# Kernel tuning notes

Hardware: AMD Instinct MI355X
Metric: run time of the kernel (lower is better)

The kernel has to match this reference:

```python
import jax, jax.numpy as jnp
import numpy as np

N_NODES = 100000


def _gcn_norm(edge_index, edge_weight, num_nodes):
    # add self loops with weight 1 (PyG GCNConv default)
    loop = jnp.arange(num_nodes, dtype=edge_index.dtype)
    src = jnp.concatenate([edge_index[0], loop])
    dst = jnp.concatenate([edge_index[1], loop])
    w = jnp.concatenate([edge_weight, jnp.ones(num_nodes, edge_weight.dtype)])
    deg = jax.ops.segment_sum(w, dst, num_segments=num_nodes)
    dinv = jnp.where(deg > 0, jax.lax.rsqrt(deg), 0.0).astype(edge_weight.dtype)
    norm = dinv[src] * w * dinv[dst]
    return src, dst, norm


def _gcn_conv(x, W, b, src, dst, norm):
    h = x @ W                                   # [N, out]
    msg = h[src] * norm[:, None]                # [E+N, out] gather + scale
    out = jax.ops.segment_sum(msg, dst, num_segments=x.shape[0])
    return out + b


def setup_inputs() -> dict:
    key = jax.random.key(0)
    ks = jax.random.split(key, 6)
    nfeat, nhid, nclass, E = 128, 64, 40, 1600000
    return {
        "x": jax.random.normal(ks[0], (N_NODES, nfeat), jnp.float32),
        "edge_index": jax.random.randint(ks[1], (2, E), 0, N_NODES, jnp.int64),
        "edge_weight": jax.random.uniform(ks[2], (E,), jnp.float32),
        "W1": jax.random.normal(ks[3], (nfeat, nhid), jnp.float32) / np.sqrt(nfeat),
        "b1": jnp.zeros((nhid,), jnp.float32),
        "W2": jax.random.normal(ks[4], (nhid, nclass), jnp.float32) / np.sqrt(nhid),
        "b2": jnp.zeros((nclass,), jnp.float32),
    }


def reference(x, edge_index, edge_weight, W1, b1, W2, b2):
    src, dst, norm = _gcn_norm(edge_index, edge_weight, x.shape[0])
    h = jax.nn.relu(_gcn_conv(x, W1, b1, src, dst, norm))
    # dropout p=0.0 / eval mode -> identity
    h = _gcn_conv(h, W2, b2, src, dst, norm)
    return jax.nn.log_softmax(h, axis=1)
```

## Files before the change

kernel.cpp:

```cpp
#include <hip/hip_runtime.h>
#include <hip/hip_fp16.h>
#include <math.h>

#define NFEAT 128
#define NHID 64
#define NCLASS 40
#define BNODES 256
#define BSHIFT 8
#define EPB 4096
#define CAPSH 13
#define CAP (1 << CAPSH)
#define LCAP 5120

typedef _Float16 f16x8 __attribute__((ext_vector_type(8)));
typedef float f32x4 __attribute__((ext_vector_type(4)));

static __device__ __forceinline__ __half2 i2h2(int x) { union { int i; __half2 h; } u; u.i = x; return u.h; }
static __device__ __forceinline__ int h22i(__half2 h) { union { int i; __half2 h; } u; u.h = h; return u.i; }
static __device__ __forceinline__ __half2 shfl_xor_h2(__half2 v, int off) { return i2h2(__shfl_xor(h22i(v), off)); }


__global__ void k_init(int* __restrict__ gcur, int NB) {
    int i = blockIdx.x * blockDim.x + threadIdx.x;
    if (i < NB) gcur[i] = i << CAPSH;
}

__global__ __launch_bounds__(256) void k_bscatter(const int* __restrict__ src, const int* __restrict__ dst,
                                                  const float* __restrict__ w, int* __restrict__ gcur,
                                                  int2* __restrict__ csrT, int E, int NB) {
    __shared__ int2 sorted[EPB];
    __shared__ int gidx[EPB];
    __shared__ int lcnt[512], lscan[512], fb[512], lpos[512];
    int t = threadIdx.x;
    for (int i = t; i < 512; i += 256) { lcnt[i] = 0; lpos[i] = 0; }
    __syncthreads();
    int base = blockIdx.x * EPB;
    int rs[16], rd[16]; float rw[16];
    #pragma unroll
    for (int j = 0; j < 4; j++) {
        int e0 = base + j * 1024 + t * 4;
        if (e0 + 3 < E) {
            int4 s4 = *(const int4*)(src + e0);
            int4 d4 = *(const int4*)(dst + e0);
            float4 w4 = *(const float4*)(w + e0);
            rs[j * 4 + 0] = s4.x; rs[j * 4 + 1] = s4.y; rs[j * 4 + 2] = s4.z; rs[j * 4 + 3] = s4.w;
            rd[j * 4 + 0] = d4.x; rd[j * 4 + 1] = d4.y; rd[j * 4 + 2] = d4.z; rd[j * 4 + 3] = d4.w;
            rw[j * 4 + 0] = w4.x; rw[j * 4 + 1] = w4.y; rw[j * 4 + 2] = w4.z; rw[j * 4 + 3] = w4.w;
        } else {
            #pragma unroll
            for (int k = 0; k < 4; k++) {
                int e = e0 + k;
                bool ok = (e < E);
                rd[j * 4 + k] = ok ? dst[e] : -1;
                rs[j * 4 + k] = ok ? src[e] : 0;
                rw[j * 4 + k] = ok ? w[e] : 0.f;
            }
        }
    }
    #pragma unroll
    for (int i = 0; i < 16; i++)
        if (rd[i] >= 0) atomicAdd(&lcnt[rd[i] >> BSHIFT], 1);
    __syncthreads();
    int i0 = t, i1 = t + 256;
    lscan[i0] = lcnt[i0]; lscan[i1] = lcnt[i1];
    __syncthreads();
    for (int off = 1; off < 512; off <<= 1) {
        int v0 = (i0 >= off) ? lscan[i0 - off] : 0;
        int v1 = (i1 >= off) ? lscan[i1 - off] : 0;
        __syncthreads();
        lscan[i0] += v0; lscan[i1] += v1;
        __syncthreads();
    }
    for (int i = t; i < NB; i += 256) {
        int c = lcnt[i];
        if (c) {
            int gb = atomicAdd(&gcur[i], c);
            fb[i] = gb - (lscan[i] - c);
        }
    }
    __syncthreads();
    #pragma unroll
    for (int i = 0; i < 16; i++) {
        if (rd[i] >= 0) {
            int d = rd[i];
            int b = d >> BSHIFT;
            int p = (lscan[b] - lcnt[b]) + atomicAdd(&lpos[b], 1);
            int2 v;
            v.x = rs[i] | ((d & (BNODES - 1)) << 20);
            v.y = __float_as_int(rw[i]);
            sorted[p] = v;
            gidx[p] = fb[b] + p;
        }
    }
    __syncthreads();
    int tot = lscan[511];
    for (int i = t; i < tot; i += 256) csrT[gidx[i]] = sorted[i];
}

__global__ __launch_bounds__(256) void k_lsort(const int* __restrict__ gcur,
                                               int2* csr,
                                               int* __restrict__ offs, int* __restrict__ endo,
                                               float* __restrict__ dinv, int N) {
    __shared__ int2 sorted[LCAP];
    __shared__ int lh[BNODES];
    __shared__ int lo[BNODES];
    __shared__ float da[BNODES];
    int b = blockIdx.x, t = threadIdx.x;
    int rbase = b << CAPSH;
    int cnt = gcur[b] - rbase;
    if (cnt > LCAP) cnt = LCAP;
    lh[t] = 0; da[t] = 0.f;
    __syncthreads();
    int2 reg[20];
    #pragma unroll
    for (int i = 0; i < 20; i++) {
        int e = t + i * 256;
        reg[i] = (e < cnt) ? csr[rbase + e] : make_int2(-1, 0);
    }
    #pragma unroll
    for (int i = 0; i < 20; i++) {
        if (reg[i].x >= 0) {
            int dl = (reg[i].x >> 20) & 255;
            atomicAdd(&lh[dl], 1);
            atomicAdd(&da[dl], __int_as_float(reg[i].y));
        }
    }
    __syncthreads();
    int own = lh[t];
    lo[t] = own;
    __syncthreads();
    for (int off = 1; off < 256; off <<= 1) {
        int v = (t >= off) ? lo[t - off] : 0;
        __syncthreads();
        lo[t] += v;
        __syncthreads();
    }
    int excl = lo[t] - own;
    __syncthreads();
    lh[t] = excl;
    int gn = (b << BSHIFT) + t;
    if (gn < N) {
        offs[gn] = rbase + excl;
        endo[gn] = rbase + excl + own;
        dinv[gn] = rsqrtf(1.0f + da[t]);
    }
    __syncthreads();
    #pragma unroll
    for (int i = 0; i < 20; i++) {
        if (reg[i].x >= 0) {
            int dl = (reg[i].x >> 20) & 255;
            int p = atomicAdd(&lh[dl], 1);
            sorted[p] = reg[i];
        }
    }
    __syncthreads();
    for (int e = t; e < cnt; e += 256) {
        int2 v = sorted[e];
        __half2 w2 = __half2half2(__float2half(__int_as_float(v.y)));
        v.x &= 0xFFFFF;
        v.y = h22i(w2);
        csr[rbase + e] = v;
    }
}


__global__ __launch_bounds__(256) void k_gemm1(const float* __restrict__ x,
                                               const float* __restrict__ W,
                                               const float* __restrict__ dinv,
                                               __half* __restrict__ h, int N) {
    __shared__ _Float16 xh[64][136];
    __shared__ _Float16 Wt[64][136];
    int t = threadIdx.x;
    int row0 = blockIdx.x * 64;
    for (int i = t; i < 2048; i += 256) {
        int r = i >> 5, k4 = i & 31;
        int row = row0 + r;
        float4 v = (row < N) ? ((const float4*)(x + (size_t)row * NFEAT))[k4]
                             : make_float4(0.f, 0.f, 0.f, 0.f);
        *(__half2*)&xh[r][k4 * 4]     = __floats2half2_rn(v.x, v.y);
        *(__half2*)&xh[r][k4 * 4 + 2] = __floats2half2_rn(v.z, v.w);
    }
    for (int i = t; i < 4096; i += 256) {
        int k2 = i >> 6, c = i & 63;
        float a0 = W[(size_t)(2 * k2) * NHID + c];
        float a1 = W[(size_t)(2 * k2 + 1) * NHID + c];
        *(__half2*)&Wt[c][k2 * 2] = __floats2half2_rn(a0, a1);
    }
    __syncthreads();
    int wave = t >> 6, lane = t & 63;
    int quad = lane >> 4, l16 = lane & 15;
    int r0 = wave * 16;
    f32x4 acc[4] = {};
    #pragma unroll
    for (int k0 = 0; k0 < 128; k0 += 32) {
        f16x8 af = *(const f16x8*)&xh[r0 + l16][k0 + quad * 8];
        #pragma unroll
        for (int ct = 0; ct < 4; ct++) {
            f16x8 bf = *(const f16x8*)&Wt[ct * 16 + l16][k0 + quad * 8];
            acc[ct] = __builtin_amdgcn_mfma_f32_16x16x32_f16(af, bf, acc[ct], 0, 0, 0);
        }
    }
    #pragma unroll
    for (int ct = 0; ct < 4; ct++) {
        #pragma unroll
        for (int j = 0; j < 4; j++) {
            int row = row0 + r0 + quad * 4 + j;
            if (row < N)
                h[(size_t)row * NHID + ct * 16 + l16] = __float2half(dinv[row] * acc[ct][j]);
        }
    }
}


__global__ __launch_bounds__(256) void k_agg1(const int* __restrict__ offs, const int* __restrict__ endo,
                                              const int2* __restrict__ csr,
                                              const __half* __restrict__ h1, const float* __restrict__ dinv,
                                              const float* __restrict__ b1, __half* __restrict__ out1, int N) {
    int n = (blockIdx.x * blockDim.x + threadIdx.x) >> 6;
    if (n >= N) return;
    int lane = threadIdx.x & 63;
    int grp = lane >> 3;
    int c8 = lane & 7;
    const char* hb = (const char*)h1;
    unsigned int c16 = (unsigned int)c8 << 4;
    int e = offs[n], end = endo[n];
    float di = dinv[n];
    float4 hsv = *(const float4*)(hb + (unsigned int)n * 128u + c16);
    float4 bb0 = ((const float4*)b1)[2 * c8];
    float4 bb1 = ((const float4*)b1)[2 * c8 + 1];
    __half2 z = __floats2half2_rn(0.f, 0.f);
    __half2 aa0[4] = {z, z, z, z}, aa1[4] = {z, z, z, z};
    __half2 aa2[4] = {z, z, z, z}, aa3[4] = {z, z, z, z};
    {
        int2 v0, v1, v2, v3;
        int i0 = e + grp, i1 = e + 8 + grp, i2 = e + 16 + grp, i3 = e + 24 + grp;
        bool b0 = i0 < end, b1v = i1 < end, b2 = i2 < end, b3 = i3 < end;
        v0 = csr[b0 ? i0 : e];
        v1 = csr[b1v ? i1 : e];
        v2 = csr[b2 ? i2 : e];
        v3 = csr[b3 ? i3 : e];
        unsigned int r0 = b0 ? (unsigned int)(v0.x & 0xFFFFF) : 0u;
        unsigned int r1 = b1v ? (unsigned int)(v1.x & 0xFFFFF) : 0u;
        unsigned int r2 = b2 ? (unsigned int)(v2.x & 0xFFFFF) : 0u;
        unsigned int r3 = b3 ? (unsigned int)(v3.x & 0xFFFFF) : 0u;
        float4 h0 = *(const float4*)(hb + r0 * 128u + c16);
        float4 h1v = *(const float4*)(hb + r1 * 128u + c16);
        float4 h2v = *(const float4*)(hb + r2 * 128u + c16);
        float4 h3v = *(const float4*)(hb + r3 * 128u + c16);
        __half2 w0 = b0 ? i2h2(v0.y) : z;
        __half2 w1 = b1v ? i2h2(v1.y) : z;
        __half2 w2 = b2 ? i2h2(v2.y) : z;
        __half2 w3 = b3 ? i2h2(v3.y) : z;
        const __half2* p0 = (const __half2*)&h0;
        const __half2* p1 = (const __half2*)&h1v;
        const __half2* p2 = (const __half2*)&h2v;
        const __half2* p3 = (const __half2*)&h3v;
        #pragma unroll
        for (int q = 0; q < 4; q++) {
            aa0[q] = __hfma2(w0, p0[q], aa0[q]);
            aa1[q] = __hfma2(w1, p1[q], aa1[q]);
            aa2[q] = __hfma2(w2, p2[q], aa2[q]);
            aa3[q] = __hfma2(w3, p3[q], aa3[q]);
        }
    }
    for (int idx = e + 32 + grp; idx < end; idx += 8) {
        int2 v = csr[idx];
        unsigned int row = (unsigned int)(v.x & 0xFFFFF);
        float4 hv = *(const float4*)(hb + row * 128u + c16);
        __half2 wv = i2h2(v.y);
        const __half2* p = (const __half2*)&hv;
        #pragma unroll
        for (int q = 0; q < 4; q++) aa0[q] = __hfma2(wv, p[q], aa0[q]);
    }
    __half2 acc2[4];
    #pragma unroll
    for (int q = 0; q < 4; q++)
        acc2[q] = __hadd2(__hadd2(aa0[q], aa1[q]), __hadd2(aa2[q], aa3[q]));
    #pragma unroll
    for (int off = 8; off <= 32; off <<= 1) {
        #pragma unroll
        for (int q = 0; q < 4; q++) acc2[q] = __hadd2(acc2[q], shfl_xor_h2(acc2[q], off));
    }
    if (grp == 0) {
        float a[8], s[8];
        #pragma unroll
        for (int q = 0; q < 4; q++) {
            float2 fa = __half22float2(acc2[q]);
            a[2 * q] = fa.x; a[2 * q + 1] = fa.y;
            float2 f = __half22float2(((const __half2*)&hsv)[q]);
            s[2 * q] = f.x; s[2 * q + 1] = f.y;
        }
        float o[8];
        o[0] = fmaxf(di * (a[0] + s[0]) + bb0.x, 0.f);
        o[1] = fmaxf(di * (a[1] + s[1]) + bb0.y, 0.f);
        o[2] = fmaxf(di * (a[2] + s[2]) + bb0.z, 0.f);
        o[3] = fmaxf(di * (a[3] + s[3]) + bb0.w, 0.f);
        o[4] = fmaxf(di * (a[4] + s[4]) + bb1.x, 0.f);
        o[5] = fmaxf(di * (a[5] + s[5]) + bb1.y, 0.f);
        o[6] = fmaxf(di * (a[6] + s[6]) + bb1.z, 0.f);
        o[7] = fmaxf(di * (a[7] + s[7]) + bb1.w, 0.f);
        float4 st;
        #pragma unroll
        for (int q = 0; q < 4; q++)
            ((__half2*)&st)[q] = __floats2half2_rn(o[2 * q], o[2 * q + 1]);
        ((float4*)out1)[(size_t)n * 8 + c8] = st;
    }
}


__global__ __launch_bounds__(256) void k_gemm2(const __half* __restrict__ a,
                                               const float* __restrict__ W,
                                               const float* __restrict__ dinv,
                                               __half* __restrict__ h, int N) {
    __shared__ _Float16 As[64][72];
    __shared__ _Float16 Bt[64][72];
    int t = threadIdx.x;
    int row0 = blockIdx.x * 64;
    for (int i = t; i < 512; i += 256) {
        int r = i >> 3, q = i & 7;
        int row = row0 + r;
        f16x8 v = {};
        if (row < N) v = *(const f16x8*)(a + (size_t)row * NHID + q * 8);
        *(f16x8*)&As[r][q * 8] = v;
    }
    for (int i = t; i < 4096; i += 256) {
        int c = i >> 6, k = i & 63;
        float wv = (c < NCLASS) ? W[k * NCLASS + c] : 0.f;
        Bt[c][k] = (_Float16)wv;
    }
    __syncthreads();
    int wave = t >> 6, lane = t & 63;
    int quad = lane >> 4, l16 = lane & 15;
    int r0 = wave * 16;
    f32x4 acc[4] = {};
    #pragma unroll
    for (int k0 = 0; k0 < 64; k0 += 32) {
        f16x8 af = *(const f16x8*)&As[r0 + l16][k0 + quad * 8];
        #pragma unroll
        for (int ct = 0; ct < 4; ct++) {
            f16x8 bf = *(const f16x8*)&Bt[ct * 16 + l16][k0 + quad * 8];
            acc[ct] = __builtin_amdgcn_mfma_f32_16x16x32_f16(af, bf, acc[ct], 0, 0, 0);
        }
    }
    #pragma unroll
    for (int ct = 0; ct < 4; ct++) {
        int col = ct * 16 + l16;
        #pragma unroll
        for (int j = 0; j < 4; j++) {
            int row = row0 + r0 + quad * 4 + j;
            if (row < N)
                h[((size_t)row << 6) + col] = __float2half(dinv[row] * acc[ct][j]);
        }
    }
}


__global__ __launch_bounds__(256) void k_agg2(const int* __restrict__ offs, const int* __restrict__ endo,
                                              const int2* __restrict__ csr,
                                              const __half* __restrict__ h2, const float* __restrict__ dinv,
                                              const float* __restrict__ b2, float* __restrict__ out, int N) {
    int n = (blockIdx.x * blockDim.x + threadIdx.x) >> 6;
    if (n >= N) return;
    int lane = threadIdx.x & 63;
    int grp = lane >> 3;
    int c8 = lane & 7;
    const char* hb = (const char*)h2;
    unsigned int c16 = (unsigned int)c8 << 4;
    int e = offs[n], end = endo[n];
    bool act = (c8 < 5);
    float di = dinv[n];
    float4 hsv = *(const float4*)(hb + ((unsigned int)n << 7) + c16);
    float4 bb0 = {}, bb1 = {};
    if (act) {
        bb0 = ((const float4*)b2)[2 * c8];
        bb1 = ((const float4*)b2)[2 * c8 + 1];
    }
    __half2 z = __floats2half2_rn(0.f, 0.f);
    __half2 aa0[4] = {z, z, z, z}, aa1[4] = {z, z, z, z};
    __half2 aa2[4] = {z, z, z, z}, aa3[4] = {z, z, z, z};
    {
        int2 v0, v1, v2, v3;
        int i0 = e + grp, i1 = e + 8 + grp, i2 = e + 16 + grp, i3 = e + 24 + grp;
        bool b0 = i0 < end, b1v = i1 < end, b2c = i2 < end, b3 = i3 < end;
        v0 = csr[b0 ? i0 : e];
        v1 = csr[b1v ? i1 : e];
        v2 = csr[b2c ? i2 : e];
        v3 = csr[b3 ? i3 : e];
        unsigned int r0 = b0 ? (unsigned int)(v0.x & 0xFFFFF) : 0u;
        unsigned int r1 = b1v ? (unsigned int)(v1.x & 0xFFFFF) : 0u;
        unsigned int r2 = b2c ? (unsigned int)(v2.x & 0xFFFFF) : 0u;
        unsigned int r3 = b3 ? (unsigned int)(v3.x & 0xFFFFF) : 0u;
        float4 h0 = *(const float4*)(hb + (r0 << 7) + c16);
        float4 h1v = *(const float4*)(hb + (r1 << 7) + c16);
        float4 h2v = *(const float4*)(hb + (r2 << 7) + c16);
        float4 h3v = *(const float4*)(hb + (r3 << 7) + c16);
        __half2 w0 = b0 ? i2h2(v0.y) : z;
        __half2 w1 = b1v ? i2h2(v1.y) : z;
        __half2 w2 = b2c ? i2h2(v2.y) : z;
        __half2 w3 = b3 ? i2h2(v3.y) : z;
        const __half2* p0 = (const __half2*)&h0;
        const __half2* p1 = (const __half2*)&h1v;
        const __half2* p2 = (const __half2*)&h2v;
        const __half2* p3 = (const __half2*)&h3v;
        #pragma unroll
        for (int q = 0; q < 4; q++) {
            aa0[q] = __hfma2(w0, p0[q], aa0[q]);
            aa1[q] = __hfma2(w1, p1[q], aa1[q]);
            aa2[q] = __hfma2(w2, p2[q], aa2[q]);
            aa3[q] = __hfma2(w3, p3[q], aa3[q]);
        }
    }
    for (int idx = e + 32 + grp; idx < end; idx += 8) {
        int2 v = csr[idx];
        unsigned int row = (unsigned int)(v.x & 0xFFFFF);
        float4 hv = *(const float4*)(hb + (row << 7) + c16);
        __half2 wv = i2h2(v.y);
        const __half2* p = (const __half2*)&hv;
        #pragma unroll
        for (int q = 0; q < 4; q++) aa0[q] = __hfma2(wv, p[q], aa0[q]);
    }
    __half2 acc2[4];
    #pragma unroll
    for (int q = 0; q < 4; q++)
        acc2[q] = __hadd2(__hadd2(aa0[q], aa1[q]), __hadd2(aa2[q], aa3[q]));
    #pragma unroll
    for (int off = 8; off <= 32; off <<= 1) {
        #pragma unroll
        for (int q = 0; q < 4; q++) acc2[q] = __hadd2(acc2[q], shfl_xor_h2(acc2[q], off));
    }
    float a[8], s[8];
    #pragma unroll
    for (int q = 0; q < 4; q++) {
        float2 fa = __half22float2(acc2[q]);
        a[2 * q] = fa.x; a[2 * q + 1] = fa.y;
        float2 f = __half22float2(((const __half2*)&hsv)[q]);
        s[2 * q] = f.x; s[2 * q + 1] = f.y;
    }
    float v[8];
    v[0] = di * (a[0] + s[0]) + bb0.x;
    v[1] = di * (a[1] + s[1]) + bb0.y;
    v[2] = di * (a[2] + s[2]) + bb0.z;
    v[3] = di * (a[3] + s[3]) + bb0.w;
    v[4] = di * (a[4] + s[4]) + bb1.x;
    v[5] = di * (a[5] + s[5]) + bb1.y;
    v[6] = di * (a[6] + s[6]) + bb1.z;
    v[7] = di * (a[7] + s[7]) + bb1.w;
    float m = -INFINITY;
    if (act) {
        #pragma unroll
        for (int k = 0; k < 8; k++) m = fmaxf(m, v[k]);
    }
    #pragma unroll
    for (int off = 1; off <= 4; off <<= 1) m = fmaxf(m, __shfl_xor(m, off));
    float ex = 0.f;
    if (act) {
        #pragma unroll
        for (int k = 0; k < 8; k++) ex += __expf(v[k] - m);
    }
    #pragma unroll
    for (int off = 1; off <= 4; off <<= 1) ex += __shfl_xor(ex, off);
    if (act && grp == 0) {
        float ls = __logf(ex);
        float4 o0, o1;
        o0.x = v[0] - m - ls; o0.y = v[1] - m - ls; o0.z = v[2] - m - ls; o0.w = v[3] - m - ls;
        o1.x = v[4] - m - ls; o1.y = v[5] - m - ls; o1.z = v[6] - m - ls; o1.w = v[7] - m - ls;
        float* op = out + (size_t)n * NCLASS + c8 * 8;
        *(float4*)op = o0;
        *(float4*)(op + 4) = o1;
    }
}


extern "C" void kernel_launch(void* const* d_in, const int* in_sizes, int n_in,
                              void* d_out, int out_size, void* d_ws, size_t ws_size,
                              hipStream_t stream) {
    const float* x  = (const float*)d_in[0];
    const int*   ei = (const int*)d_in[1];
    const float* w  = (const float*)d_in[2];
    const float* W1 = (const float*)d_in[3];
    const float* b1 = (const float*)d_in[4];
    const float* W2 = (const float*)d_in[5];
    const float* b2 = (const float*)d_in[6];
    float* out = (float*)d_out;

    const int N = in_sizes[0] / NFEAT;
    const int E = in_sizes[1] / 2;
    const int* src = ei;
    const int* dst = ei + E;

    const int NB = (N + BNODES - 1) >> BSHIFT;
    const int nbuild = (E + EPB - 1) / EPB;

    int2*   csr   = (int2*)d_ws;
    __half* h2p   = (__half*)(csr + (size_t)NB * CAP);
    float*  dinv  = (float*)(h2p + (size_t)N * 64);
    int*    offs  = (int*)(dinv + N);
    int*    endo  = offs + N;
    __half* h1h   = (__half*)(endo + N);
    __half* out1h = h1h + (size_t)N * NHID;
    int*    gcur  = (int*)(out1h + (size_t)N * NHID);

    k_init<<<(NB + 255) / 256, 256, 0, stream>>>(gcur, NB);
    k_bscatter<<<nbuild, 256, 0, stream>>>(src, dst, w, gcur, csr, E, NB);
    k_lsort<<<NB, 256, 0, stream>>>(gcur, csr, offs, endo, dinv, N);

    k_gemm1<<<(N + 63) / 64, 256, 0, stream>>>(x, W1, dinv, h1h, N);
    k_agg1<<<(N + 3) / 4, 256, 0, stream>>>(offs, endo, csr, h1h, dinv, b1, out1h, N);

    k_gemm2<<<(N + 63) / 64, 256, 0, stream>>>(out1h, W2, dinv, h2p, N);
    k_agg2<<<(N + 3) / 4, 256, 0, stream>>>(offs, endo, csr, h2p, dinv, b2, out, N);
}
```

Measured before the change: 254.9 us.

## Aggregate two nodes per wavefront with deeper edge prefetch and packed offsets

The aggregation kernels now assign 32 lanes per node instead of 64, so each wavefront handles two destination nodes. Each lane group prefetches 8 CSR entries up front before gathering, and the cross-group reduction shrinks to two shuffle steps. Row start and end offsets are packed into one int2 array so a single load fetches both. The aim is to cut idle lanes on the average 17-edge nodes and expose more memory-level parallelism, at the cost of more registers and extra loads on padded slots.

```diff
diff --git a/kernel.cpp b/kernel.cpp
--- a/kernel.cpp
+++ b/kernel.cpp
@@ -99,7 +99,7 @@
 
 __global__ __launch_bounds__(256) void k_lsort(const int* __restrict__ gcur,
                                                int2* csr,
-                                               int* __restrict__ offs, int* __restrict__ endo,
+                                               int2* __restrict__ oe,
                                                float* __restrict__ dinv, int N) {
     __shared__ int2 sorted[LCAP];
     __shared__ int lh[BNODES];
@@ -140,8 +140,7 @@
     lh[t] = excl;
     int gn = (b << BSHIFT) + t;
     if (gn < N) {
-        offs[gn] = rbase + excl;
-        endo[gn] = rbase + excl + own;
+        oe[gn] = make_int2(rbase + excl, rbase + excl + own);
         dinv[gn] = rsqrtf(1.0f + da[t]);
     }
     __syncthreads();
@@ -212,76 +211,64 @@
 }
 
 
-__global__ __launch_bounds__(256) void k_agg1(const int* __restrict__ offs, const int* __restrict__ endo,
+__global__ __launch_bounds__(256) void k_agg1(const int2* __restrict__ oe,
                                               const int2* __restrict__ csr,
                                               const __half* __restrict__ h1, const float* __restrict__ dinv,
                                               const float* __restrict__ b1, __half* __restrict__ out1, int N) {
-    int n = (blockIdx.x * blockDim.x + threadIdx.x) >> 6;
-    if (n >= N) return;
-    int lane = threadIdx.x & 63;
-    int grp = lane >> 3;
+    int t = threadIdx.x;
+    int lane = t & 63;
+    int half = lane >> 5;
+    int n = (blockIdx.x * blockDim.x + t) >> 5;
+    bool valid = n < N;
+    int nn = valid ? n : (N - 1);
+    int grp = (lane >> 3) & 3;
     int c8 = lane & 7;
     const char* hb = (const char*)h1;
     unsigned int c16 = (unsigned int)c8 << 4;
-    int e = offs[n], end = endo[n];
-    float di = dinv[n];
-    float4 hsv = *(const float4*)(hb + (unsigned int)n * 128u + c16);
+    int2 eo = oe[nn];
+    int e = eo.x, end = eo.y;
+    float di = dinv[nn];
+    float4 hsv = *(const float4*)(hb + (unsigned int)nn * 128u + c16);
     float4 bb0 = ((const float4*)b1)[2 * c8];
     float4 bb1 = ((const float4*)b1)[2 * c8 + 1];
     __half2 z = __floats2half2_rn(0.f, 0.f);
-    __half2 aa0[4] = {z, z, z, z}, aa1[4] = {z, z, z, z};
-    __half2 aa2[4] = {z, z, z, z}, aa3[4] = {z, z, z, z};
-    {
-        int2 v0, v1, v2, v3;
-        int i0 = e + grp, i1 = e + 8 + grp, i2 = e + 16 + grp, i3 = e + 24 + grp;
-        bool b0 = i0 < end, b1v = i1 < end, b2 = i2 < end, b3 = i3 < end;
-        v0 = csr[b0 ? i0 : e];
-        v1 = csr[b1v ? i1 : e];
-        v2 = csr[b2 ? i2 : e];
-        v3 = csr[b3 ? i3 : e];
-        unsigned int r0 = b0 ? (unsigned int)(v0.x & 0xFFFFF) : 0u;
-        unsigned int r1 = b1v ? (unsigned int)(v1.x & 0xFFFFF) : 0u;
-        unsigned int r2 = b2 ? (unsigned int)(v2.x & 0xFFFFF) : 0u;
-        unsigned int r3 = b3 ? (unsigned int)(v3.x & 0xFFFFF) : 0u;
-        float4 h0 = *(const float4*)(hb + r0 * 128u + c16);
-        float4 h1v = *(const float4*)(hb + r1 * 128u + c16);
-        float4 h2v = *(const float4*)(hb + r2 * 128u + c16);
-        float4 h3v = *(const float4*)(hb + r3 * 128u + c16);
-        __half2 w0 = b0 ? i2h2(v0.y) : z;
-        __half2 w1 = b1v ? i2h2(v1.y) : z;
-        __half2 w2 = b2 ? i2h2(v2.y) : z;
-        __half2 w3 = b3 ? i2h2(v3.y) : z;
-        const __half2* p0 = (const __half2*)&h0;
-        const __half2* p1 = (const __half2*)&h1v;
-        const __half2* p2 = (const __half2*)&h2v;
-        const __half2* p3 = (const __half2*)&h3v;
-        #pragma unroll
-        for (int q = 0; q < 4; q++) {
-            aa0[q] = __hfma2(w0, p0[q], aa0[q]);
-            aa1[q] = __hfma2(w1, p1[q], aa1[q]);
-            aa2[q] = __hfma2(w2, p2[q], aa2[q]);
-            aa3[q] = __hfma2(w3, p3[q], aa3[q]);
-        }
-    }
-    for (int idx = e + 32 + grp; idx < end; idx += 8) {
+    __half2 aa[4][4] = {{z,z,z,z},{z,z,z,z},{z,z,z,z},{z,z,z,z}};
+    int2 cv[8];
+    #pragma unroll
+    for (int r = 0; r < 8; r++) {
+        int idx = e + r * 4 + grp;
+        cv[r] = csr[idx < end ? idx : e];
+    }
+    #pragma unroll
+    for (int r = 0; r < 8; r++) {
+        int idx = e + r * 4 + grp;
+        bool ok = idx < end;
+        unsigned int row = ok ? (unsigned int)(cv[r].x & 0xFFFFF) : 0u;
+        float4 hv = *(const float4*)(hb + row * 128u + c16);
+        __half2 wv = ok ? i2h2(cv[r].y) : z;
+        const __half2* p = (const __half2*)&hv;
+        #pragma unroll
+        for (int q = 0; q < 4; q++) aa[r & 3][q] = __hfma2(wv, p[q], aa[r & 3][q]);
+    }
+    for (int idx = e + 32 + grp; idx < end; idx += 4) {
         int2 v = csr[idx];
         unsigned int row = (unsigned int)(v.x & 0xFFFFF);
         float4 hv = *(const float4*)(hb + row * 128u + c16);
         __half2 wv = i2h2(v.y);
         const __half2* p = (const __half2*)&hv;
         #pragma unroll
-        for (int q = 0; q < 4; q++) aa0[q] = __hfma2(wv, p[q], aa0[q]);
+        for (int q = 0; q < 4; q++) aa[0][q] = __hfma2(wv, p[q], aa[0][q]);
     }
     __half2 acc2[4];
     #pragma unroll
     for (int q = 0; q < 4; q++)
-        acc2[q] = __hadd2(__hadd2(aa0[q], aa1[q]), __hadd2(aa2[q], aa3[q]));
-    #pragma unroll
-    for (int off = 8; off <= 32; off <<= 1) {
+        acc2[q] = __hadd2(__hadd2(aa[0][q], aa[1][q]), __hadd2(aa[2][q], aa[3][q]));
+    #pragma unroll
+    for (int off = 8; off <= 16; off <<= 1) {
         #pragma unroll
         for (int q = 0; q < 4; q++) acc2[q] = __hadd2(acc2[q], shfl_xor_h2(acc2[q], off));
     }
-    if (grp == 0) {
+    if (valid && grp == 0) {
         float a[8], s[8];
         #pragma unroll
         for (int q = 0; q < 4; q++) {
@@ -355,76 +342,63 @@
 }
 
 
-__global__ __launch_bounds__(256) void k_agg2(const int* __restrict__ offs, const int* __restrict__ endo,
+__global__ __launch_bounds__(256) void k_agg2(const int2* __restrict__ oe,
                                               const int2* __restrict__ csr,
                                               const __half* __restrict__ h2, const float* __restrict__ dinv,
                                               const float* __restrict__ b2, float* __restrict__ out, int N) {
-    int n = (blockIdx.x * blockDim.x + threadIdx.x) >> 6;
-    if (n >= N) return;
-    int lane = threadIdx.x & 63;
-    int grp = lane >> 3;
+    int t = threadIdx.x;
+    int lane = t & 63;
+    int n = (blockIdx.x * blockDim.x + t) >> 5;
+    bool valid = n < N;
+    int nn = valid ? n : (N - 1);
+    int grp = (lane >> 3) & 3;
     int c8 = lane & 7;
     const char* hb = (const char*)h2;
     unsigned int c16 = (unsigned int)c8 << 4;
-    int e = offs[n], end = endo[n];
+    int2 eo = oe[nn];
+    int e = eo.x, end = eo.y;
     bool act = (c8 < 5);
-    float di = dinv[n];
-    float4 hsv = *(const float4*)(hb + ((unsigned int)n << 7) + c16);
+    float di = dinv[nn];
+    float4 hsv = *(const float4*)(hb + ((unsigned int)nn << 7) + c16);
     float4 bb0 = {}, bb1 = {};
     if (act) {
         bb0 = ((const float4*)b2)[2 * c8];
         bb1 = ((const float4*)b2)[2 * c8 + 1];
     }
     __half2 z = __floats2half2_rn(0.f, 0.f);
-    __half2 aa0[4] = {z, z, z, z}, aa1[4] = {z, z, z, z};
-    __half2 aa2[4] = {z, z, z, z}, aa3[4] = {z, z, z, z};
-    {
-        int2 v0, v1, v2, v3;
-        int i0 = e + grp, i1 = e + 8 + grp, i2 = e + 16 + grp, i3 = e + 24 + grp;
-        bool b0 = i0 < end, b1v = i1 < end, b2c = i2 < end, b3 = i3 < end;
-        v0 = csr[b0 ? i0 : e];
-        v1 = csr[b1v ? i1 : e];
-        v2 = csr[b2c ? i2 : e];
-        v3 = csr[b3 ? i3 : e];
-        unsigned int r0 = b0 ? (unsigned int)(v0.x & 0xFFFFF) : 0u;
-        unsigned int r1 = b1v ? (unsigned int)(v1.x & 0xFFFFF) : 0u;
-        unsigned int r2 = b2c ? (unsigned int)(v2.x & 0xFFFFF) : 0u;
-        unsigned int r3 = b3 ? (unsigned int)(v3.x & 0xFFFFF) : 0u;
-        float4 h0 = *(const float4*)(hb + (r0 << 7) + c16);
-        float4 h1v = *(const float4*)(hb + (r1 << 7) + c16);
-        float4 h2v = *(const float4*)(hb + (r2 << 7) + c16);
-        float4 h3v = *(const float4*)(hb + (r3 << 7) + c16);
-        __half2 w0 = b0 ? i2h2(v0.y) : z;
-        __half2 w1 = b1v ? i2h2(v1.y) : z;
-        __half2 w2 = b2c ? i2h2(v2.y) : z;
-        __half2 w3 = b3 ? i2h2(v3.y) : z;
-        const __half2* p0 = (const __half2*)&h0;
-        const __half2* p1 = (const __half2*)&h1v;
-        const __half2* p2 = (const __half2*)&h2v;
-        const __half2* p3 = (const __half2*)&h3v;
-        #pragma unroll
-        for (int q = 0; q < 4; q++) {
-            aa0[q] = __hfma2(w0, p0[q], aa0[q]);
-            aa1[q] = __hfma2(w1, p1[q], aa1[q]);
-            aa2[q] = __hfma2(w2, p2[q], aa2[q]);
-            aa3[q] = __hfma2(w3, p3[q], aa3[q]);
-        }
-    }
-    for (int idx = e + 32 + grp; idx < end; idx += 8) {
+    __half2 aa[4][4] = {{z,z,z,z},{z,z,z,z},{z,z,z,z},{z,z,z,z}};
+    int2 cv[8];
+    #pragma unroll
+    for (int r = 0; r < 8; r++) {
+        int idx = e + r * 4 + grp;
+        cv[r] = csr[idx < end ? idx : e];
+    }
+    #pragma unroll
+    for (int r = 0; r < 8; r++) {
+        int idx = e + r * 4 + grp;
+        bool ok = idx < end;
+        unsigned int row = ok ? (unsigned int)(cv[r].x & 0xFFFFF) : 0u;
+        float4 hv = *(const float4*)(hb + (row << 7) + c16);
+        __half2 wv = ok ? i2h2(cv[r].y) : z;
+        const __half2* p = (const __half2*)&hv;
+        #pragma unroll
+        for (int q = 0; q < 4; q++) aa[r & 3][q] = __hfma2(wv, p[q], aa[r & 3][q]);
+    }
+    for (int idx = e + 32 + grp; idx < end; idx += 4) {
         int2 v = csr[idx];
         unsigned int row = (unsigned int)(v.x & 0xFFFFF);
         float4 hv = *(const float4*)(hb + (row << 7) + c16);
         __half2 wv = i2h2(v.y);
         const __half2* p = (const __half2*)&hv;
         #pragma unroll
-        for (int q = 0; q < 4; q++) aa0[q] = __hfma2(wv, p[q], aa0[q]);
+        for (int q = 0; q < 4; q++) aa[0][q] = __hfma2(wv, p[q], aa[0][q]);
     }
     __half2 acc2[4];
     #pragma unroll
     for (int q = 0; q < 4; q++)
-        acc2[q] = __hadd2(__hadd2(aa0[q], aa1[q]), __hadd2(aa2[q], aa3[q]));
-    #pragma unroll
-    for (int off = 8; off <= 32; off <<= 1) {
+        acc2[q] = __hadd2(__hadd2(aa[0][q], aa[1][q]), __hadd2(aa[2][q], aa[3][q]));
+    #pragma unroll
+    for (int off = 8; off <= 16; off <<= 1) {
         #pragma unroll
         for (int q = 0; q < 4; q++) acc2[q] = __hadd2(acc2[q], shfl_xor_h2(acc2[q], off));
     }
@@ -459,7 +433,7 @@
     }
     #pragma unroll
     for (int off = 1; off <= 4; off <<= 1) ex += __shfl_xor(ex, off);
-    if (act && grp == 0) {
+    if (valid && act && grp == 0) {
         float ls = __logf(ex);
         float4 o0, o1;
         o0.x = v[0] - m - ls; o0.y = v[1] - m - ls; o0.z = v[2] - m - ls; o0.w = v[3] - m - ls;
@@ -494,19 +468,18 @@
     int2*   csr   = (int2*)d_ws;
     __half* h2p   = (__half*)(csr + (size_t)NB * CAP);
     float*  dinv  = (float*)(h2p + (size_t)N * 64);
-    int*    offs  = (int*)(dinv + N);
-    int*    endo  = offs + N;
-    __half* h1h   = (__half*)(endo + N);
+    int2*   oe    = (int2*)(dinv + N);
+    __half* h1h   = (__half*)(oe + N);
     __half* out1h = h1h + (size_t)N * NHID;
     int*    gcur  = (int*)(out1h + (size_t)N * NHID);
 
     k_init<<<(NB + 255) / 256, 256, 0, stream>>>(gcur, NB);
     k_bscatter<<<nbuild, 256, 0, stream>>>(src, dst, w, gcur, csr, E, NB);
-    k_lsort<<<NB, 256, 0, stream>>>(gcur, csr, offs, endo, dinv, N);
+    k_lsort<<<NB, 256, 0, stream>>>(gcur, csr, oe, dinv, N);
 
     k_gemm1<<<(N + 63) / 64, 256, 0, stream>>>(x, W1, dinv, h1h, N);
-    k_agg1<<<(N + 3) / 4, 256, 0, stream>>>(offs, endo, csr, h1h, dinv, b1, out1h, N);
+    k_agg1<<<(N + 7) / 8, 256, 0, stream>>>(oe, csr, h1h, dinv, b1, out1h, N);
 
     k_gemm2<<<(N + 63) / 64, 256, 0, stream>>>(out1h, W2, dinv, h2p, N);
-    k_agg2<<<(N + 3) / 4, 256, 0, stream>>>(offs, endo, csr, h2p, dinv, b2, out, N);
-}
+    k_agg2<<<(N + 7) / 8, 256, 0, stream>>>(oe, csr, h2p, dinv, b2, out, N);
+}
```

New measurement: 243.3 us. -4.5%, faster.
